# Performance work log

Measured on AMD Instinct MI355X. Metric: run time of the kernel, lower is better.

Reference implementation:

```python
import jax, jax.numpy as jnp
import numpy as np

N_RES = 512
N_POINT = 512
C = 128  # c_p == c_z == c_hidden == c_pz (required by the source's gating linears)
EPS = 1e-5


def _ln(x, w, b):
    m = jnp.mean(x, axis=-1, keepdims=True)
    v = jnp.mean(jnp.square(x - m), axis=-1, keepdims=True)
    return (x - m) * jax.lax.rsqrt(v + EPS) * w + b


def _lin(x, w, b):
    # w: [out, in] (torch convention)
    return jnp.einsum('...i,oi->...o', x, w) + b


def setup_inputs() -> dict:
    key = jax.random.key(0)
    ks = jax.random.split(key, 16)
    s = 0.02
    return {
        'z': jax.random.normal(ks[0], (N_RES, N_RES, C), jnp.float32),
        'p': jax.random.normal(ks[1], (N_POINT, N_POINT, C), jnp.float32),
        'mask': jnp.ones((N_RES, N_RES), jnp.float32),
        'w_lp': jax.random.normal(ks[2], (C, C), jnp.float32) * s,
        'b_lp': jnp.zeros((C,), jnp.float32),
        'w_rp': jax.random.normal(ks[3], (C, C), jnp.float32) * s,
        'b_rp': jnp.zeros((C,), jnp.float32),
        'w_lg': jax.random.normal(ks[4], (C, C), jnp.float32) * s,
        'b_lg': jnp.ones((C,), jnp.float32),   # 'gating' init: bias=1
        'w_rg': jax.random.normal(ks[5], (C, C), jnp.float32) * s,
        'b_rg': jnp.ones((C,), jnp.float32),
        'w_z': jax.random.normal(ks[6], (C, C), jnp.float32) * s,
        'b_z': jnp.zeros((C,), jnp.float32),
        'ln_l_w': jnp.ones((C,), jnp.float32),
        'ln_l_b': jnp.zeros((C,), jnp.float32),
        'ln_r_w': jnp.ones((C,), jnp.float32),
        'ln_r_b': jnp.zeros((C,), jnp.float32),
        'ln_o_w': jnp.ones((C,), jnp.float32),
        'ln_o_b': jnp.zeros((C,), jnp.float32),
    }


def reference(z, p, mask, w_lp, b_lp, w_rp, b_rp, w_lg, b_lg, w_rg, b_rg,
              w_z, b_z, ln_l_w, ln_l_b, ln_r_w, ln_r_b, ln_o_w, ln_o_b):
    m = mask[..., None]                       # [N_res, N_res, 1]
    x_l = _lin(_ln(p, ln_l_w, ln_l_b), w_lp, b_lp)          # [N_pt, N_pt, C]
    x_r = m * _lin(_ln(z, ln_r_w, ln_r_b), w_rp, b_rp)      # [N_res, N_res, C]
    g_l = jax.nn.sigmoid(_lin(x_l, w_lg, b_lg))
    g_r = jax.nn.sigmoid(_lin(x_r, w_rg, b_rg))
    x_l = g_l * x_l
    x_r = g_r * x_r
    # outcomming: sum over j (second-to-last spatial axis)
    z_l = jnp.sum(x_l, axis=-2)               # [N_pt, C]
    z_r = jnp.sum(x_r, axis=-2)               # [N_res, C]
    out = z_l[..., :, None, :] * z_r[..., None, :, :]        # [N_pt, N_res, C]
    return _lin(_ln(out, ln_o_w, ln_o_b), w_z, b_z)
```

## Files before the change

### kernel.cpp

```cpp
#include <hip/hip_runtime.h>
#include <hip/hip_bf16.h>
#include <math.h>

#define NRES 512
#define CC   128
#define LN_EPS 1e-5f
#define SPLIT_SCALE 1024.0f
#define SPLIT_INV   0.0009765625f

typedef _Float16 half_t;
typedef __attribute__((ext_vector_type(8))) _Float16 f16x8;
typedef __attribute__((ext_vector_type(4))) float f32x4;

__device__ __forceinline__ float sigmoidf_(float x) {
    return 1.0f / (1.0f + __expf(-x));
}

__global__ __launch_bounds__(512)
void phaseA_kernel(const float* __restrict__ p, const float* __restrict__ z,
                   const float* __restrict__ mask,
                   const float* __restrict__ Wlp, const float* __restrict__ blp,
                   const float* __restrict__ Wlg, const float* __restrict__ blg,
                   const float* __restrict__ Wrp, const float* __restrict__ brp,
                   const float* __restrict__ Wrg, const float* __restrict__ brg,
                   const float* __restrict__ lnlw, const float* __restrict__ lnlb,
                   const float* __restrict__ lnrw, const float* __restrict__ lnrb,
                   float* __restrict__ SL)
{
    __shared__ __align__(16) half_t sWp_hi[CC*CC];
    __shared__ __align__(16) half_t sWp_lo[CC*CC];
    __shared__ __align__(16) half_t sWg  [CC*CC];
    __shared__ __align__(16) half_t sAX  [128*CC];
    __shared__ float sbp[CC], sbg[CC], slnw[CC], slnb[CC];
    __shared__ float smask[NRES];
    __shared__ float sred[8][CC];

    const int t    = threadIdx.x;
    const int side = blockIdx.x >> 8;
    const int i0   = blockIdx.x & 255;
    const int lane = t & 63;
    const int w    = t >> 6;

    const float* X   = side ? z   : p;
    const float* Wp  = side ? Wrp : Wlp;
    const float* bp  = side ? brp : blp;
    const float* Wg  = side ? Wrg : Wlg;
    const float* bg  = side ? brg : blg;
    const float* lnw = side ? lnrw : lnlw;
    const float* lnb = side ? lnrb : lnlb;
    const bool   use_mask = (side != 0);

    {
        const int o = t >> 2, q = t & 3;
        const float* wp_row = Wp + o * CC;
        const float* wg_row = Wg + o * CC;
        #pragma unroll
        for (int b = 0; b < 4; ++b) {
            const int blk  = q * 4 + b;
            const int dblk = blk ^ (o & 7);
            f32x4 lo  = *(const f32x4*)(wp_row + blk*8);
            f32x4 hi  = *(const f32x4*)(wp_row + blk*8 + 4);
            f32x4 lo2 = *(const f32x4*)(wg_row + blk*8);
            f32x4 hi2 = *(const f32x4*)(wg_row + blk*8 + 4);
            f16x8 vh, vl, vg;
            #pragma unroll
            for (int e = 0; e < 4; ++e) {
                float w0 = lo[e], w1 = hi[e];
                half_t h0 = (half_t)w0, h1 = (half_t)w1;
                vh[e] = h0; vh[e+4] = h1;
                vl[e]   = (half_t)((w0 - (float)h0) * SPLIT_SCALE);
                vl[e+4] = (half_t)((w1 - (float)h1) * SPLIT_SCALE);
                vg[e]   = (half_t)lo2[e]; vg[e+4] = (half_t)hi2[e];
            }
            *(f16x8*)&sWp_hi[o*CC + dblk*8] = vh;
            *(f16x8*)&sWp_lo[o*CC + dblk*8] = vl;
            *(f16x8*)&sWg  [o*CC + dblk*8] = vg;
        }
    }
    if (t < CC) { sbp[t] = bp[t]; sbg[t] = bg[t]; slnw[t] = lnw[t]; slnb[t] = lnb[t]; }

    const int r     = t >> 2;
    const int q     = t & 3;
    const int kq    = lane >> 4;
    const int arow  = (w << 4) + (lane & 15);
    const int drow0 = (w << 4) + (kq << 2);

    for (int ii = 0; ii < 2; ++ii) {
        const int i = i0 + (ii << 8);

        if (use_mask) {
            for (int j = t; j < NRES; j += 512) smask[j] = mask[(size_t)i*NRES + j];
        }
        __syncthreads();

        float colacc[8];
        #pragma unroll
        for (int c = 0; c < 8; ++c) colacc[c] = 0.f;

        for (int chunk = 0; chunk < 4; ++chunk) {
            const int j0 = chunk * 128;

            f16x8 alo_sv[4];
            {
                const float* rowp = X + ((size_t)i*NRES + (j0 + r)) * CC + q*32;
                float vals[32];
                float sum = 0.f, sq = 0.f;
                #pragma unroll
                for (int k = 0; k < 8; ++k) {
                    f32x4 v4 = *(const f32x4*)(rowp + k*4);
                    #pragma unroll
                    for (int e = 0; e < 4; ++e) {
                        float x = v4[e];
                        vals[k*4+e] = x;
                        sum += x; sq += x*x;
                    }
                }
                sum += __shfl_xor(sum, 1); sum += __shfl_xor(sum, 2);
                sq  += __shfl_xor(sq , 1); sq  += __shfl_xor(sq , 2);
                const float m  = sum * (1.f/CC);
                const float rs = rsqrtf(sq * (1.f/CC) - m*m + LN_EPS);
                #pragma unroll
                for (int b = 0; b < 4; ++b) {
                    f16x8 o8;
                    #pragma unroll
                    for (int e = 0; e < 8; ++e) {
                        const int c = q*32 + b*8 + e;
                        float lnv = (vals[b*8+e] - m) * rs * slnw[c] + slnb[c];
                        half_t h = (half_t)lnv;
                        o8[e] = h;
                        alo_sv[b][e] = (half_t)((lnv - (float)h) * SPLIT_SCALE);
                    }
                    *(f16x8*)&sAX[r*CC + ((q*4+b) ^ (r & 7))*8] = o8;
                }
            }
            __syncthreads();

            f16x8 afh[4];
            #pragma unroll
            for (int kk = 0; kk < 4; ++kk)
                afh[kk] = *(const f16x8*)&sAX[arow*CC + (((kk<<2)+kq) ^ (arow & 7))*8];
            __syncthreads();

            #pragma unroll
            for (int b = 0; b < 4; ++b)
                *(f16x8*)&sAX[r*CC + ((q*4+b) ^ (r & 7))*8] = alo_sv[b];
            __syncthreads();

            f16x8 afl[4];
            #pragma unroll
            for (int kk = 0; kk < 4; ++kk)
                afl[kk] = *(const f16x8*)&sAX[arow*CC + (((kk<<2)+kq) ^ (arow & 7))*8];
            __syncthreads();

            float xv[8][4];
            float mrow[4];
            if (use_mask) {
                #pragma unroll
                for (int rr = 0; rr < 4; ++rr) mrow[rr] = smask[j0 + drow0 + rr];
            }
            #pragma unroll
            for (int ct = 0; ct < 8; ++ct) {
                const int ocol = (ct << 4) + (lane & 15);
                f32x4 acc1 = {0.f,0.f,0.f,0.f};
                f32x4 acc2 = {0.f,0.f,0.f,0.f};
                #pragma unroll
                for (int kk = 0; kk < 4; ++kk) {
                    const int idx = ocol*CC + (((kk<<2)+kq) ^ (ocol & 7))*8;
                    f16x8 whi = *(const f16x8*)&sWp_hi[idx];
                    f16x8 wlo = *(const f16x8*)&sWp_lo[idx];
                    acc1 = __builtin_amdgcn_mfma_f32_16x16x32_f16(afh[kk], whi, acc1, 0, 0, 0);
                    acc2 = __builtin_amdgcn_mfma_f32_16x16x32_f16(afh[kk], wlo, acc2, 0, 0, 0);
                    acc2 = __builtin_amdgcn_mfma_f32_16x16x32_f16(afl[kk], whi, acc2, 0, 0, 0);
                }
                const float bias = sbp[ocol];
                #pragma unroll
                for (int rr = 0; rr < 4; ++rr) {
                    float x = acc1[rr] + acc2[rr]*SPLIT_INV + bias;
                    if (use_mask) x *= mrow[rr];
                    xv[ct][rr] = x;
                    const int dr = drow0 + rr;
                    sAX[dr*CC + (((ocol>>3) ^ (dr & 7))<<3) + (ocol & 7)] = (half_t)x;
                }
            }
            __syncthreads();

            f16x8 a2[4];
            #pragma unroll
            for (int kk = 0; kk < 4; ++kk)
                a2[kk] = *(const f16x8*)&sAX[arow*CC + (((kk<<2)+kq) ^ (arow & 7))*8];
            #pragma unroll
            for (int ct = 0; ct < 8; ++ct) {
                const int ocol = (ct << 4) + (lane & 15);
                f32x4 acc = {0.f,0.f,0.f,0.f};
                #pragma unroll
                for (int kk = 0; kk < 4; ++kk) {
                    f16x8 bfr = *(const f16x8*)&sWg[ocol*CC + (((kk<<2)+kq) ^ (ocol & 7))*8];
                    acc = __builtin_amdgcn_mfma_f32_16x16x32_f16(a2[kk], bfr, acc, 0, 0, 0);
                }
                const float bias = sbg[ocol];
                float part = 0.f;
                #pragma unroll
                for (int rr = 0; rr < 4; ++rr)
                    part += sigmoidf_(acc[rr] + bias) * xv[ct][rr];
                part += __shfl_xor(part, 16);
                part += __shfl_xor(part, 32);
                colacc[ct] += part;
            }
            __syncthreads();
        }

        if (lane < 16) {
            #pragma unroll
            for (int ct = 0; ct < 8; ++ct) sred[w][(ct<<4) + lane] = colacc[ct];
        }
        __syncthreads();
        if (t < CC) {
            float s = 0.f;
            #pragma unroll
            for (int ww = 0; ww < 8; ++ww) s += sred[ww][t];
            SL[((size_t)side*NRES + i)*CC + t] = s;
        }
    }
}

__global__ __launch_bounds__(512, 4)
void phaseB_kernel(const float* __restrict__ zl, const float* __restrict__ zr,
                   const float* __restrict__ Wz, const float* __restrict__ bz,
                   const float* __restrict__ lnw, const float* __restrict__ lnb,
                   float* __restrict__ out)
{
    __shared__ __align__(16) half_t sW_hi[CC*CC];
    __shared__ __align__(16) half_t sAX[128*CC];
    __shared__ float szl[CC], sbz[CC], slnw[CC], slnb[CC];

    const int t    = threadIdx.x;
    const int i    = blockIdx.x;
    const int lane = t & 63;
    const int w    = t >> 6;

    {
        const int o = t >> 2, q = t & 3;
        const float* wrow = Wz + o * CC;
        #pragma unroll
        for (int b = 0; b < 4; ++b) {
            const int blk  = q*4 + b;
            const int dblk = blk ^ (o & 7);
            f32x4 lo = *(const f32x4*)(wrow + blk*8);
            f32x4 hi = *(const f32x4*)(wrow + blk*8 + 4);
            f16x8 vh;
            #pragma unroll
            for (int e = 0; e < 4; ++e) {
                vh[e] = (half_t)lo[e]; vh[e+4] = (half_t)hi[e];
            }
            *(f16x8*)&sW_hi[o*CC + dblk*8] = vh;
        }
    }
    if (t < CC) { szl[t] = zl[(size_t)i*CC + t]; sbz[t] = bz[t]; slnw[t] = lnw[t]; slnb[t] = lnb[t]; }
    __syncthreads();

    const int kq    = lane >> 4;
    const int arow  = (w << 4) + (lane & 15);
    const int drow0 = (w << 4) + (kq << 2);

    for (int chunk = 0; chunk < 4; ++chunk) {
        const int j0 = chunk * 128;

        {
            const int r = t >> 2, q = t & 3;
            const float* rowp = zr + (size_t)(j0 + r) * CC + q*32;
            float vals[32];
            float sum = 0.f, sq = 0.f;
            #pragma unroll
            for (int k = 0; k < 8; ++k) {
                f32x4 v4 = *(const f32x4*)(rowp + k*4);
                #pragma unroll
                for (int e = 0; e < 4; ++e) {
                    float x = v4[e] * szl[q*32 + k*4 + e];
                    vals[k*4+e] = x;
                    sum += x; sq += x*x;
                }
            }
            sum += __shfl_xor(sum, 1); sum += __shfl_xor(sum, 2);
            sq  += __shfl_xor(sq , 1); sq  += __shfl_xor(sq , 2);
            const float m  = sum * (1.f/CC);
            const float rs = rsqrtf(sq * (1.f/CC) - m*m + LN_EPS);
            #pragma unroll
            for (int b = 0; b < 4; ++b) {
                f16x8 o8;
                #pragma unroll
                for (int e = 0; e < 8; ++e) {
                    const int c = q*32 + b*8 + e;
                    o8[e] = (half_t)((vals[b*8+e] - m) * rs * slnw[c] + slnb[c]);
                }
                *(f16x8*)&sAX[r*CC + ((q*4+b) ^ (r & 7))*8] = o8;
            }
        }
        __syncthreads();

        f16x8 afh[4];
        #pragma unroll
        for (int kk = 0; kk < 4; ++kk)
            afh[kk] = *(const f16x8*)&sAX[arow*CC + (((kk<<2)+kq) ^ (arow & 7))*8];

        #pragma unroll
        for (int ct = 0; ct < 8; ++ct) {
            const int ocol = (ct << 4) + (lane & 15);
            f32x4 acc1 = {0.f,0.f,0.f,0.f};
            #pragma unroll
            for (int kk = 0; kk < 4; ++kk) {
                const int idx = ocol*CC + (((kk<<2)+kq) ^ (ocol & 7))*8;
                f16x8 whi = *(const f16x8*)&sW_hi[idx];
                acc1 = __builtin_amdgcn_mfma_f32_16x16x32_f16(afh[kk], whi, acc1, 0, 0, 0);
            }
            const float bias = sbz[ocol];
            #pragma unroll
            for (int rr = 0; rr < 4; ++rr) {
                const size_t j = (size_t)(j0 + drow0 + rr);
                out[((size_t)i*NRES + j)*CC + ocol] = acc1[rr] + bias;
            }
        }
        __syncthreads();
    }
}

extern "C" void kernel_launch(void* const* d_in, const int* in_sizes, int n_in,
                              void* d_out, int out_size, void* d_ws, size_t ws_size,
                              hipStream_t stream)
{
    (void)in_sizes; (void)n_in; (void)out_size; (void)ws_size;
    const float* z      = (const float*)d_in[0];
    const float* p      = (const float*)d_in[1];
    const float* mask   = (const float*)d_in[2];
    const float* w_lp   = (const float*)d_in[3];
    const float* b_lp   = (const float*)d_in[4];
    const float* w_rp   = (const float*)d_in[5];
    const float* b_rp   = (const float*)d_in[6];
    const float* w_lg   = (const float*)d_in[7];
    const float* b_lg   = (const float*)d_in[8];
    const float* w_rg   = (const float*)d_in[9];
    const float* b_rg   = (const float*)d_in[10];
    const float* w_z    = (const float*)d_in[11];
    const float* b_z    = (const float*)d_in[12];
    const float* ln_l_w = (const float*)d_in[13];
    const float* ln_l_b = (const float*)d_in[14];
    const float* ln_r_w = (const float*)d_in[15];
    const float* ln_r_b = (const float*)d_in[16];
    const float* ln_o_w = (const float*)d_in[17];
    const float* ln_o_b = (const float*)d_in[18];
    float* out = (float*)d_out;

    float* zl = (float*)d_ws;
    float* zr = zl + NRES*CC;

    phaseA_kernel<<<dim3(2*256), dim3(512), 0, stream>>>(
        p, z, mask, w_lp, b_lp, w_lg, b_lg, w_rp, b_rp, w_rg, b_rg,
        ln_l_w, ln_l_b, ln_r_w, ln_r_b, zl);

    phaseB_kernel<<<dim3(NRES), dim3(512), 0, stream>>>(
        zl, zr, w_z, b_z, ln_o_w, ln_o_b, out);
}
```

Measured before the change: 258.1 us.

## Pad shared-memory row stride and halve phase A grid with four rows per block

Pads the shared-memory row stride of the f16 weight and activation tiles from 128 to 144 elements in both kernels, on top of the existing XOR swizzle, to change LDS bank mapping. Phase A now launches 256 blocks, each handling four rows of one side instead of two. This spreads the weight conversion into LDS over more rows but lowers parallelism to one block per CU. The padding also raises LDS use per block, which could limit occupancy.

```diff
diff --git a/kernel.cpp b/kernel.cpp
--- a/kernel.cpp
+++ b/kernel.cpp
@@ -4,6 +4,7 @@
 
 #define NRES 512
 #define CC   128
+#define SROW 144
 #define LN_EPS 1e-5f
 #define SPLIT_SCALE 1024.0f
 #define SPLIT_INV   0.0009765625f
@@ -27,17 +28,17 @@
                    const float* __restrict__ lnrw, const float* __restrict__ lnrb,
                    float* __restrict__ SL)
 {
-    __shared__ __align__(16) half_t sWp_hi[CC*CC];
-    __shared__ __align__(16) half_t sWp_lo[CC*CC];
-    __shared__ __align__(16) half_t sWg  [CC*CC];
-    __shared__ __align__(16) half_t sAX  [128*CC];
+    __shared__ __align__(16) half_t sWp_hi[CC*SROW];
+    __shared__ __align__(16) half_t sWp_lo[CC*SROW];
+    __shared__ __align__(16) half_t sWg  [CC*SROW];
+    __shared__ __align__(16) half_t sAX  [128*SROW];
     __shared__ float sbp[CC], sbg[CC], slnw[CC], slnb[CC];
     __shared__ float smask[NRES];
     __shared__ float sred[8][CC];
 
     const int t    = threadIdx.x;
-    const int side = blockIdx.x >> 8;
-    const int i0   = blockIdx.x & 255;
+    const int side = blockIdx.x >> 7;
+    const int i0   = blockIdx.x & 127;
     const int lane = t & 63;
     const int w    = t >> 6;
 
@@ -72,9 +73,9 @@
                 vl[e+4] = (half_t)((w1 - (float)h1) * SPLIT_SCALE);
                 vg[e]   = (half_t)lo2[e]; vg[e+4] = (half_t)hi2[e];
             }
-            *(f16x8*)&sWp_hi[o*CC + dblk*8] = vh;
-            *(f16x8*)&sWp_lo[o*CC + dblk*8] = vl;
-            *(f16x8*)&sWg  [o*CC + dblk*8] = vg;
+            *(f16x8*)&sWp_hi[o*SROW + dblk*8] = vh;
+            *(f16x8*)&sWp_lo[o*SROW + dblk*8] = vl;
+            *(f16x8*)&sWg  [o*SROW + dblk*8] = vg;
         }
     }
     if (t < CC) { sbp[t] = bp[t]; sbg[t] = bg[t]; slnw[t] = lnw[t]; slnb[t] = lnb[t]; }
@@ -85,8 +86,8 @@
     const int arow  = (w << 4) + (lane & 15);
     const int drow0 = (w << 4) + (kq << 2);
 
-    for (int ii = 0; ii < 2; ++ii) {
-        const int i = i0 + (ii << 8);
+    for (int ii = 0; ii < 4; ++ii) {
+        const int i = i0 + (ii << 7);
 
         if (use_mask) {
             for (int j = t; j < NRES; j += 512) smask[j] = mask[(size_t)i*NRES + j];
@@ -130,7 +131,7 @@
                         o8[e] = h;
                         alo_sv[b][e] = (half_t)((lnv - (float)h) * SPLIT_SCALE);
                     }
-                    *(f16x8*)&sAX[r*CC + ((q*4+b) ^ (r & 7))*8] = o8;
+                    *(f16x8*)&sAX[r*SROW + ((q*4+b) ^ (r & 7))*8] = o8;
                 }
             }
             __syncthreads();
@@ -138,18 +139,18 @@
             f16x8 afh[4];
             #pragma unroll
             for (int kk = 0; kk < 4; ++kk)
-                afh[kk] = *(const f16x8*)&sAX[arow*CC + (((kk<<2)+kq) ^ (arow & 7))*8];
+                afh[kk] = *(const f16x8*)&sAX[arow*SROW + (((kk<<2)+kq) ^ (arow & 7))*8];
             __syncthreads();
 
             #pragma unroll
             for (int b = 0; b < 4; ++b)
-                *(f16x8*)&sAX[r*CC + ((q*4+b) ^ (r & 7))*8] = alo_sv[b];
+                *(f16x8*)&sAX[r*SROW + ((q*4+b) ^ (r & 7))*8] = alo_sv[b];
             __syncthreads();
 
             f16x8 afl[4];
             #pragma unroll
             for (int kk = 0; kk < 4; ++kk)
-                afl[kk] = *(const f16x8*)&sAX[arow*CC + (((kk<<2)+kq) ^ (arow & 7))*8];
+                afl[kk] = *(const f16x8*)&sAX[arow*SROW + (((kk<<2)+kq) ^ (arow & 7))*8];
             __syncthreads();
 
             float xv[8][4];
@@ -165,7 +166,7 @@
                 f32x4 acc2 = {0.f,0.f,0.f,0.f};
                 #pragma unroll
                 for (int kk = 0; kk < 4; ++kk) {
-                    const int idx = ocol*CC + (((kk<<2)+kq) ^ (ocol & 7))*8;
+                    const int idx = ocol*SROW + (((kk<<2)+kq) ^ (ocol & 7))*8;
                     f16x8 whi = *(const f16x8*)&sWp_hi[idx];
                     f16x8 wlo = *(const f16x8*)&sWp_lo[idx];
                     acc1 = __builtin_amdgcn_mfma_f32_16x16x32_f16(afh[kk], whi, acc1, 0, 0, 0);
@@ -179,7 +180,7 @@
                     if (use_mask) x *= mrow[rr];
                     xv[ct][rr] = x;
                     const int dr = drow0 + rr;
-                    sAX[dr*CC + (((ocol>>3) ^ (dr & 7))<<3) + (ocol & 7)] = (half_t)x;
+                    sAX[dr*SROW + (((ocol>>3) ^ (dr & 7))<<3) + (ocol & 7)] = (half_t)x;
                 }
             }
             __syncthreads();
@@ -187,14 +188,14 @@
             f16x8 a2[4];
             #pragma unroll
             for (int kk = 0; kk < 4; ++kk)
-                a2[kk] = *(const f16x8*)&sAX[arow*CC + (((kk<<2)+kq) ^ (arow & 7))*8];
+                a2[kk] = *(const f16x8*)&sAX[arow*SROW + (((kk<<2)+kq) ^ (arow & 7))*8];
             #pragma unroll
             for (int ct = 0; ct < 8; ++ct) {
                 const int ocol = (ct << 4) + (lane & 15);
                 f32x4 acc = {0.f,0.f,0.f,0.f};
                 #pragma unroll
                 for (int kk = 0; kk < 4; ++kk) {
-                    f16x8 bfr = *(const f16x8*)&sWg[ocol*CC + (((kk<<2)+kq) ^ (ocol & 7))*8];
+                    f16x8 bfr = *(const f16x8*)&sWg[ocol*SROW + (((kk<<2)+kq) ^ (ocol & 7))*8];
                     acc = __builtin_amdgcn_mfma_f32_16x16x32_f16(a2[kk], bfr, acc, 0, 0, 0);
                 }
                 const float bias = sbg[ocol];
@@ -229,8 +230,8 @@
                    const float* __restrict__ lnw, const float* __restrict__ lnb,
                    float* __restrict__ out)
 {
-    __shared__ __align__(16) half_t sW_hi[CC*CC];
-    __shared__ __align__(16) half_t sAX[128*CC];
+    __shared__ __align__(16) half_t sW_hi[CC*SROW];
+    __shared__ __align__(16) half_t sAX[128*SROW];
     __shared__ float szl[CC], sbz[CC], slnw[CC], slnb[CC];
 
     const int t    = threadIdx.x;
@@ -252,7 +253,7 @@
             for (int e = 0; e < 4; ++e) {
                 vh[e] = (half_t)lo[e]; vh[e+4] = (half_t)hi[e];
             }
-            *(f16x8*)&sW_hi[o*CC + dblk*8] = vh;
+            *(f16x8*)&sW_hi[o*SROW + dblk*8] = vh;
         }
     }
     if (t < CC) { szl[t] = zl[(size_t)i*CC + t]; sbz[t] = bz[t]; slnw[t] = lnw[t]; slnb[t] = lnb[t]; }
@@ -292,7 +293,7 @@
                     const int c = q*32 + b*8 + e;
                     o8[e] = (half_t)((vals[b*8+e] - m) * rs * slnw[c] + slnb[c]);
                 }
-                *(f16x8*)&sAX[r*CC + ((q*4+b) ^ (r & 7))*8] = o8;
+                *(f16x8*)&sAX[r*SROW + ((q*4+b) ^ (r & 7))*8] = o8;
             }
         }
         __syncthreads();
@@ -300,7 +301,7 @@
         f16x8 afh[4];
         #pragma unroll
         for (int kk = 0; kk < 4; ++kk)
-            afh[kk] = *(const f16x8*)&sAX[arow*CC + (((kk<<2)+kq) ^ (arow & 7))*8];
+            afh[kk] = *(const f16x8*)&sAX[arow*SROW + (((kk<<2)+kq) ^ (arow & 7))*8];
 
         #pragma unroll
         for (int ct = 0; ct < 8; ++ct) {
@@ -308,7 +309,7 @@
             f32x4 acc1 = {0.f,0.f,0.f,0.f};
             #pragma unroll
             for (int kk = 0; kk < 4; ++kk) {
-                const int idx = ocol*CC + (((kk<<2)+kq) ^ (ocol & 7))*8;
+                const int idx = ocol*SROW + (((kk<<2)+kq) ^ (ocol & 7))*8;
                 f16x8 whi = *(const f16x8*)&sW_hi[idx];
                 acc1 = __builtin_amdgcn_mfma_f32_16x16x32_f16(afh[kk], whi, acc1, 0, 0, 0);
             }
@@ -352,7 +353,7 @@
     float* zl = (float*)d_ws;
     float* zr = zl + NRES*CC;
 
-    phaseA_kernel<<<dim3(2*256), dim3(512), 0, stream>>>(
+    phaseA_kernel<<<dim3(256), dim3(512), 0, stream>>>(
         p, z, mask, w_lp, b_lp, w_lg, b_lg, w_rp, b_rp, w_rg, b_rg,
         ln_l_w, ln_l_b, ln_r_w, ln_r_b, zl);
 
```

After: 252.4 us. -2.2%, faster.
